# Performance work log

Measured on AMD Instinct MI355X. Metric: run time of the kernel, lower is better.

Reference implementation:

```python
import jax, jax.numpy as jnp
import numpy as np

EPS = 1e-5
AVG_D = 32.0


def setup_inputs() -> dict:
    key = jax.random.key(0)
    ks = jax.random.split(key, 12)
    Ns, Nd, E, D, K = 1_000_000, 100_000, 3_200_000, 16, 2
    Fs, Fd, V = 4, 4, 100_000
    F = Fd + K  # predictor fields
    inp = {}
    inp["Cat_src"] = jax.random.randint(ks[0], (Ns, Fs), 0, V)
    inp["Cat_dst"] = jax.random.randint(ks[1], (Nd, Fd), 0, V)
    inp["src_ids"] = jax.random.randint(ks[2], (E,), 0, Ns)
    inp["dst_ids"] = jax.random.randint(ks[3], (E,), 0, Nd)
    inp["label"] = jax.random.randint(ks[4], (Nd,), 0, 2)
    inp["w"] = jax.random.normal(ks[5], (V, D), dtype=jnp.float32) * 0.05
    inp["W_agg"] = jax.random.normal(ks[6], (K, 12 * D, D), dtype=jnp.float32) * 0.05
    inp["b_agg"] = jnp.zeros((K, D), jnp.float32)
    inp["w_lin"] = jax.random.normal(ks[7], (F * D,), dtype=jnp.float32) * 0.05
    inp["b_lin"] = jnp.zeros((1,), jnp.float32)
    inp["W1"] = jax.random.normal(ks[8], (F * D, 64), dtype=jnp.float32) * 0.05
    inp["b1"] = jnp.zeros((64,), jnp.float32)
    inp["W2"] = jax.random.normal(ks[9], (64, 32), dtype=jnp.float32) * 0.05
    inp["b2"] = jnp.zeros((32,), jnp.float32)
    inp["W3"] = jax.random.normal(ks[10], (32, 1), dtype=jnp.float32) * 0.05
    inp["b3"] = jnp.zeros((1,), jnp.float32)
    return inp


def reference(Cat_src, Cat_dst, src_ids, dst_ids, label, w, W_agg, b_agg,
              w_lin, b_lin, W1, b1, W2, b2, W3, b3):
    Nd = Cat_dst.shape[0]
    # --- node embedding: gather cat fields, RowEmb with modes [mean, max] -> [Ns, K, D]
    emb = w[Cat_src]                                      # [Ns, Fs, D]
    h_src = jnp.stack([emb.mean(1), emb.max(1)], axis=1)  # [Ns, K, D]
    # --- multi-aggregator message passing (copy_u + segment min/max/mean, std via mean of h^2)
    m = h_src[src_ids]                                    # [E, K, D]
    deg = jax.ops.segment_sum(jnp.ones(src_ids.shape, m.dtype), dst_ids, Nd)
    safe = jnp.maximum(deg, 1.0)[:, None, None]
    mean = jax.ops.segment_sum(m, dst_ids, Nd) / safe
    mean2 = jax.ops.segment_sum(m * m, dst_ids, Nd) / safe
    has = (deg > 0)[:, None, None]
    mn = jnp.where(has, jax.ops.segment_min(m, dst_ids, Nd), 0.0)
    mx = jnp.where(has, jax.ops.segment_max(m, dst_ids, Nd), 0.0)
    std = jnp.sqrt(jax.nn.relu(mean2 - mean * mean) + EPS)
    tmp = jnp.concatenate([mean, mn, mx, std], axis=-1)   # [Nd, K, 4D]
    # --- PNA degree scalers: identity / amplification / attenuation
    logd = jnp.log(deg + 1.0)
    log_avg = jnp.log(AVG_D + 1.0)
    amp = (logd / log_avg)[:, None, None]
    att = jnp.where(logd > 0, log_avg / jnp.maximum(logd, EPS), 0.0)[:, None, None]
    scaled = jnp.concatenate([tmp, tmp * amp, tmp * att], axis=-1)  # [Nd, K, 12D]
    mes = jnp.einsum('nkf,kfd->nkd', scaled, W_agg) + b_agg          # [Nd, K, D]
    # --- final block: concat dst cat embeddings with aggregated messages
    x = jnp.concatenate([w[Cat_dst], mes], axis=1)        # [Nd, F, D]
    # --- DeepFM predictor: linear + FM pairwise + deep MLP
    flat = x.reshape(Nd, -1)
    lin = flat @ w_lin + b_lin[0]
    s = x.sum(1)
    fm = 0.5 * ((s * s) - (x * x).sum(1)).sum(-1)
    h = jax.nn.relu(flat @ W1 + b1)
    h = jax.nn.relu(h @ W2 + b2)
    deep = (h @ W3 + b3)[:, 0]
    pred = jax.nn.sigmoid(lin + fm + deep)
    return (pred, label)
```

## Files before the change

### kernel.cpp

```cpp
#include <hip/hip_runtime.h>
#include <math.h>

#define EPSF 1e-5f
#define CAP  88
#define SBH  9
#define MAXSB 256
#define SBCAP 23552
#define TILE 4096
#define SEG  8
#define XPADS2 104
#define X2PADS 72
#define NPACK 14336

typedef __attribute__((ext_vector_type(8))) short short8;
typedef __attribute__((ext_vector_type(4))) float float4v;

__device__ inline unsigned f2bf_rne(float x) {
    unsigned u = __float_as_uint(x);
    u += 0x7FFF + ((u >> 16) & 1);
    return u >> 16;
}
__device__ inline short bf16_of(float x) { return (short)f2bf_rne(x); }
__device__ inline float bf2f_lo(unsigned hv) { return __uint_as_float(hv << 16); }
__device__ inline float bf2f_hi(unsigned hv) { return __uint_as_float(hv & 0xFFFF0000u); }
__device__ inline float bf2f_s(ushort s) { return __uint_as_float((unsigned)s << 16); }

__global__ __launch_bounds__(256) void setup_all(
    int* sbcursor, int* deg, int Nd, int nsb,
    const float* __restrict__ W_agg, const float* __restrict__ W1,
    const float* __restrict__ W2, ushort* __restrict__ wpack,
    const float* __restrict__ w, ushort* __restrict__ wb, int VD, int do_cast)
{
    int nzc = (Nd + 255) >> 8;
    int bid = blockIdx.x;
    if (bid < nzc) {
        int i = bid * 256 + threadIdx.x;
        if (i < Nd) deg[i] = 0;
        if (bid == 0 && threadIdx.x < nsb) sbcursor[threadIdx.x] = threadIdx.x * SBCAP;
        return;
    }
    if (bid == nzc) {
        for (int it = threadIdx.x; it < 1792; it += 256) {
            if (it < 768) {
                int t_g = it >> 6; int rem = it & 63;
                int q = rem >> 4, col = rem & 15;
                int kvar = t_g / 6, t = t_g % 6;
                const float* src = W_agg + kvar * 3072 + (t * 32 + q * 8) * 16 + col;
                ushort* dst = wpack + (size_t)it * 8;
#pragma unroll
                for (int j = 0; j < 8; ++j) dst[j] = (ushort)f2bf_rne(src[j * 16]);
            } else if (it < 1536) {
                int i2 = it - 768;
                int t = i2 >> 8; int rem = i2 & 255;
                int q = rem >> 6, col = rem & 63;
                const float* src = W1 + (t * 32 + q * 8) * 64 + col;
                ushort* dst = wpack + 6144 + (size_t)i2 * 8;
#pragma unroll
                for (int j = 0; j < 8; ++j) dst[j] = (ushort)f2bf_rne(src[j * 64]);
            } else {
                int i2 = it - 1536;
                int t = i2 >> 7; int rem = i2 & 127;
                int q = rem >> 5, col = rem & 31;
                const float* src = W2 + (t * 32 + q * 8) * 32 + col;
                ushort* dst = wpack + 12288 + (size_t)i2 * 8;
#pragma unroll
                for (int j = 0; j < 8; ++j) dst[j] = (ushort)f2bf_rne(src[j * 32]);
            }
        }
        return;
    }
    if (!do_cast) return;
    int i4 = ((bid - nzc - 1) * 256 + threadIdx.x) * 4;
    if (i4 + 3 < VD) {
        float4 v = *(const float4*)(w + i4);
        ushort4 o;
        o.x = (ushort)f2bf_rne(v.x); o.y = (ushort)f2bf_rne(v.y);
        o.z = (ushort)f2bf_rne(v.z); o.w = (ushort)f2bf_rne(v.w);
        *(ushort4*)(wb + i4) = o;
    } else {
        for (int j = i4; j < VD; ++j) wb[j] = (ushort)f2bf_rne(w[j]);
    }
}

__global__ __launch_bounds__(256) void build_h(
    const int* __restrict__ Cat_src, const ushort* __restrict__ wb,
    unsigned* __restrict__ h, int Ns)
{
    int gid = blockIdx.x * 256 + threadIdx.x;
    int s = gid >> 4;
    if (s >= Ns) return;
    int lane = threadIdx.x & 63;
    int d = lane & 15;
    int c = Cat_src[s * 4 + (d & 3)];
    float vs = 0.f, vm = -INFINITY;
#pragma unroll
    for (int f = 0; f < 4; ++f) {
        int id = __shfl(c, (lane & 48) + f, 64);
        float a = bf2f_s(wb[id * 16 + d]);
        vs += a; vm = fmaxf(vm, a);
    }
    unsigned packed = f2bf_rne(vs * 0.25f) | (f2bf_rne(vm) << 16);
    __builtin_nontemporal_store(packed, &h[s * 16 + d]);
}

__global__ __launch_bounds__(256) void scatter_sb(
    const int* __restrict__ src_ids, const int* __restrict__ dst_ids,
    int* sbcursor, unsigned* __restrict__ pairs1, int E, int nsb)
{
    __shared__ int cnt[MAXSB];
    __shared__ int base[MAXSB];
    int tid = threadIdx.x;
    int t0 = blockIdx.x * TILE;
    for (int i = tid; i < nsb; i += 256) cnt[i] = 0;
    __syncthreads();
    int rank[TILE / 256];
#pragma unroll
    for (int j = 0; j < TILE / 256; ++j) {
        int e = t0 + j * 256 + tid;
        rank[j] = (e < E) ? atomicAdd(&cnt[dst_ids[e] >> SBH], 1) : 0;
    }
    __syncthreads();
    for (int i = tid; i < nsb; i += 256) {
        int c = cnt[i];
        base[i] = c ? atomicAdd(&sbcursor[i], c) : 0;
    }
    __syncthreads();
#pragma unroll
    for (int j = 0; j < TILE / 256; ++j) {
        int e = t0 + j * 256 + tid;
        if (e < E) {
            int d = dst_ids[e];
            int sb = d >> SBH;
            int idx = base[sb] + rank[j];
            if (idx < (sb + 1) * SBCAP)
                pairs1[idx] = ((unsigned)src_ids[e] << 9) | (unsigned)(d & 511);
        }
    }
}

__global__ __launch_bounds__(256) void scatter_fine3(
    const unsigned* __restrict__ pairs1, const int* __restrict__ sbcursor,
    unsigned* __restrict__ pairs2, int* __restrict__ deg, int Nd, int nsb,
    int nsbp)
{
    __shared__ int cnt[512];
    __shared__ int base[512];
    int S = blockIdx.x % nsbp, seg = blockIdx.x / nsbp;
    if (S >= nsb) return;
    int tid = threadIdx.x;
    int sbs = S * SBCAP;
    int sbe = sbcursor[S];
    if (sbe > sbs + SBCAP) sbe = sbs + SBCAP;
    int len = sbe - sbs;
    int per = (len + SEG - 1) / SEG;
    int s0 = sbs + seg * per;
    int s1 = s0 + per; if (s1 > sbe) s1 = sbe;
    cnt[tid] = 0; cnt[tid + 256] = 0;
    __syncthreads();
    int rank[12];
    unsigned pv[12];
    int nit = (s1 - s0 + 255) >> 8;
    if (nit > 12) nit = 12;
    for (int j = 0; j < nit; ++j) {
        int e = s0 + j * 256 + tid;
        if (e < s1) {
            unsigned p = __builtin_nontemporal_load(&pairs1[e]);
            pv[j] = p;
            rank[j] = atomicAdd(&cnt[p & 511u], 1);
        }
    }
    __syncthreads();
#pragma unroll
    for (int r = 0; r < 2; ++r) {
        int l = tid + r * 256;
        int c = cnt[l];
        int gdst = (S << 9) + l;
        base[l] = (c && gdst < Nd) ? atomicAdd(&deg[gdst], c) : 0;
    }
    __syncthreads();
    for (int j = 0; j < nit; ++j) {
        int e = s0 + j * 256 + tid;
        if (e < s1) {
            unsigned p = pv[j];
            int l = (int)(p & 511u);
            int idx = base[l] + rank[j];
            if (idx < CAP)
                pairs2[(size_t)((S << 9) + l) * CAP + idx] = p >> 9;
        }
    }
}

__device__ inline void emit_stats(float sum0, float sq0, float mn0, float mx0,
                                  float sum1, float sq1, float mn1, float mx1,
                                  int dg, int n, int lane, int sub,
                                  ushort* __restrict__ tmpb)
{
#pragma unroll
    for (int off = 16; off <= 32; off <<= 1) {
        sum0 += __shfl_xor(sum0, off); sq0 += __shfl_xor(sq0, off);
        mn0 = fminf(mn0, __shfl_xor(mn0, off)); mx0 = fmaxf(mx0, __shfl_xor(mx0, off));
        sum1 += __shfl_xor(sum1, off); sq1 += __shfl_xor(sq1, off);
        mn1 = fminf(mn1, __shfl_xor(mn1, off)); mx1 = fmaxf(mx1, __shfl_xor(mx1, off));
    }
    float safe = fmaxf((float)dg, 1.f);
    float r = 1.f / safe;
    bool has = dg > 0;
    float mean0 = sum0 * r, mean1 = sum1 * r;
    float sd0 = sqrtf(fmaxf(sq0 * r - mean0 * mean0, 0.f) + EPSF);
    float sd1 = sqrtf(fmaxf(sq1 * r - mean1 * mean1, 0.f) + EPSF);
    float v0 = (sub == 0) ? mean0 : (sub == 1) ? (has ? mn0 : 0.f)
             : (sub == 2) ? (has ? mx0 : 0.f) : sd0;
    float v1 = (sub == 0) ? mean1 : (sub == 1) ? (has ? mn1 : 0.f)
             : (sub == 2) ? (has ? mx1 : 0.f) : sd1;
    ushort* tp = tmpb + (size_t)n * 128;
    tp[lane] = (ushort)f2bf_rne(v0);
    tp[64 + lane] = (ushort)f2bf_rne(v1);
}

#define ACC8(HV)  do { \
    float me = bf2f_lo(HV); \
    float vm = bf2f_hi(HV); \
    sum0 += me; sq0 += me * me; \
    mn0 = fminf(mn0, me); mx0 = fmaxf(mx0, me); \
    sum1 += vm; sq1 += vm * vm; \
    mn1 = fminf(mn1, vm); mx1 = fmaxf(mx1, vm); } while (0)

__global__ __launch_bounds__(256) void agg_from_h2(
    const unsigned* __restrict__ h, const int* __restrict__ deg,
    const unsigned* __restrict__ pairs,
    ushort* __restrict__ tmpb, int Nd)
{
    int tid = threadIdx.x;
    int wv = tid >> 6, lane = tid & 63, sub = lane >> 4, d = lane & 15;
    int n = blockIdx.x * 4 + wv;
    if (n >= Nd) return;
    int dg = deg[n];
    int dgc = (dg < CAP) ? dg : CAP;
    const unsigned* pw = pairs + (size_t)n * CAP;

    float sum0 = 0.f, sq0 = 0.f, mn0 = INFINITY, mx0 = -INFINITY;
    float sum1 = 0.f, sq1 = 0.f, mn1 = INFINITY, mx1 = -INFINITY;

    int t64 = dgc >> 6;
    for (int t = 0; t < t64; ++t) {
        const unsigned* pp = pw + t * 64 + sub;
        unsigned pv[16], hv[16];
#pragma unroll
        for (int j = 0; j < 16; ++j) pv[j] = pp[j * 4];
#pragma unroll
        for (int j = 0; j < 16; ++j) hv[j] = h[pv[j] * 16 + d];
#pragma unroll
        for (int j = 0; j < 16; ++j) ACC8(hv[j]);
    }
    int base = t64 << 6;
    if (dgc & 32) {
        const unsigned* pp = pw + base + sub;
        unsigned pv[8], hv[8];
#pragma unroll
        for (int j = 0; j < 8; ++j) pv[j] = pp[j * 4];
#pragma unroll
        for (int j = 0; j < 8; ++j) hv[j] = h[pv[j] * 16 + d];
#pragma unroll
        for (int j = 0; j < 8; ++j) ACC8(hv[j]);
        base += 32;
    }
    int rem = dgc - base;
    if (rem > 0) {
        int last = dgc - 1;
        unsigned pv[8], hv[8];
#pragma unroll
        for (int j = 0; j < 8; ++j) {
            if (j * 4 < rem) {
                int e = base + j * 4 + sub;
                pv[j] = pw[e < last ? e : last];
            }
        }
#pragma unroll
        for (int j = 0; j < 8; ++j)
            if (j * 4 < rem) hv[j] = h[pv[j] * 16 + d];
#pragma unroll
        for (int j = 0; j < 8; ++j) {
            if (j * 4 < rem) {
                if (base + j * 4 + sub < dgc) ACC8(hv[j]);
            }
        }
    }
    emit_stats(sum0, sq0, mn0, mx0, sum1, sq1, mn1, mx1,
               dg, n, lane, sub, tmpb);
}

__global__ __launch_bounds__(256) void agg_from_w2(
    const int* __restrict__ Cat_src, const float* __restrict__ w,
    const ushort* __restrict__ wb, int use_bf,
    const int* __restrict__ deg, const unsigned* __restrict__ pairs,
    ushort* __restrict__ tmpb, int Nd)
{
    int tid = threadIdx.x;
    int wv = tid >> 6, lane = tid & 63, sub = lane >> 4, d = lane & 15;
    int n = blockIdx.x * 4 + wv;
    if (n >= Nd) return;
    int dg = deg[n];
    int dgc = (dg < CAP) ? dg : CAP;
    const unsigned* pw = pairs + (size_t)n * CAP;

    float sum0 = 0.f, sq0 = 0.f, mn0 = INFINITY, mx0 = -INFINITY;
    float sum1 = 0.f, sq1 = 0.f, mn1 = INFINITY, mx1 = -INFINITY;
    int nt = (dgc + 3) >> 2;
    for (int t = 0; t < nt; ++t) {
        int e4 = t * 4 + sub;
        int ec = (e4 < dgc) ? e4 : (dgc - 1);
        int src = (int)pw[ec];
        int cat = Cat_src[src * 4 + (d & 3)];
        float vs = 0.f, vm = -INFINITY;
        if (use_bf) {
#pragma unroll
            for (int f = 0; f < 4; ++f) {
                int id = __shfl(cat, sub * 16 + f, 64);
                float a = bf2f_s(wb[id * 16 + d]);
                vs += a; vm = fmaxf(vm, a);
            }
        } else {
#pragma unroll
            for (int f = 0; f < 4; ++f) {
                int id = __shfl(cat, sub * 16 + f, 64);
                float a = w[id * 16 + d];
                vs += a; vm = fmaxf(vm, a);
            }
        }
        if (e4 < dgc) {
            float me = vs * 0.25f;
            sum0 += me; sq0 += me * me;
            mn0 = fminf(mn0, me); mx0 = fmaxf(mx0, me);
            sum1 += vm; sq1 += vm * vm;
            mn1 = fminf(mn1, vm); mx1 = fmaxf(mx1, vm);
        }
    }
    emit_stats(sum0, sq0, mn0, mx0, sum1, sq1, mn1, mx1,
               dg, n, lane, sub, tmpb);
}

__global__ __launch_bounds__(256) void finalize_mfma(
    const int* __restrict__ Cat_dst, const int* __restrict__ label,
    const float* __restrict__ w, const ushort* __restrict__ wpack,
    const float* __restrict__ b_agg,
    const float* __restrict__ w_lin, const float* __restrict__ b_lin,
    const float* __restrict__ b1, const float* __restrict__ b2,
    const float* __restrict__ W3, const float* __restrict__ b3,
    const int* __restrict__ deg_arr, const ushort* __restrict__ tmpb,
    float* __restrict__ out, int Nd)
{
    __shared__ __align__(16) ushort sx[4][16 * XPADS2];
    __shared__ __align__(16) ushort sx2[4][16 * X2PADS];
    __shared__ float sdeep[4][16];

    int tid = threadIdx.x;
    int wv = tid >> 6, lane = tid & 63;
    int q = lane >> 4, m = lane & 15;
    int n0 = (blockIdx.x * 4 + wv) * 16;
    int n = n0 + m;
    int nc = (n < Nd) ? n : (Nd - 1);

    ushort* X = sx[wv];
    ushort* X2 = sx2[wv];

    float fdeg = (float)deg_arr[nc];
    float logd = logf(fdeg + 1.f);
    const float logavg = logf(33.0f);
    float amp = logd / logavg;
    float att = (logd > 0.f) ? (logavg / fmaxf(logd, EPSF)) : 0.f;
    float ampr[4], attr[4];
#pragma unroll
    for (int r = 0; r < 4; ++r) {
        ampr[r] = __shfl(amp, q * 4 + r, 64);
        attr[r] = __shfl(att, q * 4 + r, 64);
    }

    const ushort* tpn = tmpb + (size_t)nc * 128;
#pragma unroll
    for (int kvar = 0; kvar < 2; ++kvar) {
        short8 af0 = *(const short8*)(tpn + kvar * 64 + q * 8);
        short8 af1 = *(const short8*)(tpn + kvar * 64 + 32 + q * 8);
        float4v aI = {0.f,0.f,0.f,0.f}, aA = {0.f,0.f,0.f,0.f}, aT = {0.f,0.f,0.f,0.f};
#pragma unroll
        for (int sb = 0; sb < 3; ++sb) {
            short8 b0 = *(const short8*)(wpack +
                (size_t)(((kvar * 6 + sb * 2) * 4 + q) * 16 + m) * 8);
            short8 b1v = *(const short8*)(wpack +
                (size_t)(((kvar * 6 + sb * 2 + 1) * 4 + q) * 16 + m) * 8);
            if (sb == 0) {
                aI = __builtin_amdgcn_mfma_f32_16x16x32_bf16(af0, b0, aI, 0, 0, 0);
                aI = __builtin_amdgcn_mfma_f32_16x16x32_bf16(af1, b1v, aI, 0, 0, 0);
            } else if (sb == 1) {
                aA = __builtin_amdgcn_mfma_f32_16x16x32_bf16(af0, b0, aA, 0, 0, 0);
                aA = __builtin_amdgcn_mfma_f32_16x16x32_bf16(af1, b1v, aA, 0, 0, 0);
            } else {
                aT = __builtin_amdgcn_mfma_f32_16x16x32_bf16(af0, b0, aT, 0, 0, 0);
                aT = __builtin_amdgcn_mfma_f32_16x16x32_bf16(af1, b1v, aT, 0, 0, 0);
            }
        }
        float bias = b_agg[kvar * 16 + m];
#pragma unroll
        for (int r = 0; r < 4; ++r)
            X[(q * 4 + r) * XPADS2 + 64 + kvar * 16 + m] = (ushort)f2bf_rne(
                aI[r] + ampr[r] * aA[r] + attr[r] * aT[r] + bias);
    }
    {
        int nl = lane >> 2, fl = lane & 3;
        int nn = n0 + nl;
        int nnc = (nn < Nd) ? nn : (Nd - 1);
        int cid = Cat_dst[nnc * 4 + fl];
        const float4* R = (const float4*)(w + (size_t)cid * 16);
        float4 r0 = R[0], r1 = R[1], r2 = R[2], r3 = R[3];
        short8 o0, o1;
        o0[0] = bf16_of(r0.x); o0[1] = bf16_of(r0.y);
        o0[2] = bf16_of(r0.z); o0[3] = bf16_of(r0.w);
        o0[4] = bf16_of(r1.x); o0[5] = bf16_of(r1.y);
        o0[6] = bf16_of(r1.z); o0[7] = bf16_of(r1.w);
        o1[0] = bf16_of(r2.x); o1[1] = bf16_of(r2.y);
        o1[2] = bf16_of(r2.z); o1[3] = bf16_of(r2.w);
        o1[4] = bf16_of(r3.x); o1[5] = bf16_of(r3.y);
        o1[6] = bf16_of(r3.z); o1[7] = bf16_of(r3.w);
        ushort* xp = X + nl * XPADS2 + fl * 16;
        *(short8*)(xp) = o0;
        *(short8*)(xp + 8) = o1;
    }
    __syncthreads();

    float lin = 0.f, sq = 0.f;
    float sd[16];
#pragma unroll
    for (int u = 0; u < 16; ++u) sd[u] = 0.f;
    {
        const ushort* xp = X + m * XPADS2 + q * 16;
        const float* wl = w_lin + q * 16;
#pragma unroll
        for (int u = 0; u < 16; ++u) {
            float v = bf2f_s(xp[u]);
            lin += v * wl[u]; sq += v * v; sd[u] += v;
        }
    }
    if (q < 2) {
        const ushort* xp = X + m * XPADS2 + (4 + q) * 16;
        const float* wl = w_lin + (4 + q) * 16;
#pragma unroll
        for (int u = 0; u < 16; ++u) {
            float v = bf2f_s(xp[u]);
            lin += v * wl[u]; sq += v * v; sd[u] += v;
        }
    }
#pragma unroll
    for (int off = 16; off <= 32; off <<= 1) {
        lin += __shfl_xor(lin, off);
        sq  += __shfl_xor(sq, off);
#pragma unroll
        for (int u = 0; u < 16; ++u) sd[u] += __shfl_xor(sd[u], off);
    }
    float fm = 0.f;
#pragma unroll
    for (int u = 0; u < 16; ++u) fm += sd[u] * sd[u];
    fm = 0.5f * (fm - sq);

    short8 xa[3];
#pragma unroll
    for (int t = 0; t < 3; ++t)
        xa[t] = *(const short8*)(X + m * XPADS2 + t * 32 + q * 8);
#pragma unroll
    for (int nt = 0; nt < 4; ++nt) {
        float4v acc = {0.f, 0.f, 0.f, 0.f};
#pragma unroll
        for (int t = 0; t < 3; ++t) {
            short8 bf = *(const short8*)(wpack + 6144 +
                (size_t)((t * 4 + q) * 64 + nt * 16 + m) * 8);
            acc = __builtin_amdgcn_mfma_f32_16x16x32_bf16(xa[t], bf, acc, 0, 0, 0);
        }
        float bb = b1[nt * 16 + m];
#pragma unroll
        for (int r = 0; r < 4; ++r)
            X2[(q * 4 + r) * X2PADS + nt * 16 + m] =
                (ushort)f2bf_rne(fmaxf(acc[r] + bb, 0.f));
    }
    __syncthreads();

    short8 ha[2];
#pragma unroll
    for (int t = 0; t < 2; ++t)
        ha[t] = *(const short8*)(X2 + m * X2PADS + t * 32 + q * 8);
    float dp[4] = {0.f, 0.f, 0.f, 0.f};
#pragma unroll
    for (int nt = 0; nt < 2; ++nt) {
        float4v acc = {0.f, 0.f, 0.f, 0.f};
#pragma unroll
        for (int t = 0; t < 2; ++t) {
            short8 bf = *(const short8*)(wpack + 12288 +
                (size_t)((t * 4 + q) * 32 + nt * 16 + m) * 8);
            acc = __builtin_amdgcn_mfma_f32_16x16x32_bf16(ha[t], bf, acc, 0, 0, 0);
        }
        float bb = b2[nt * 16 + m];
        float w3 = W3[nt * 16 + m];
#pragma unroll
        for (int r = 0; r < 4; ++r)
            dp[r] += fmaxf(acc[r] + bb, 0.f) * w3;
    }
#pragma unroll
    for (int off = 1; off <= 8; off <<= 1) {
#pragma unroll
        for (int r = 0; r < 4; ++r) dp[r] += __shfl_xor(dp[r], off);
    }
    if (m < 4)
        sdeep[wv][q * 4 + m] = (m == 0) ? dp[0] : (m == 1) ? dp[1]
                             : (m == 2) ? dp[2] : dp[3];
    __syncthreads();
    float deep = sdeep[wv][m];

    if (q == 0 && n < Nd) {
        float z = lin + b_lin[0] + fm + deep + b3[0];
        float pred = 1.f / (1.f + expf(-z));
        out[n] = pred;
        out[Nd + n] = (float)label[n];
    }
}

extern "C" void kernel_launch(void* const* d_in, const int* in_sizes, int n_in,
                              void* d_out, int out_size, void* d_ws, size_t ws_size,
                              hipStream_t stream) {
    const int*   Cat_src = (const int*)d_in[0];
    const int*   Cat_dst = (const int*)d_in[1];
    const int*   src_ids = (const int*)d_in[2];
    const int*   dst_ids = (const int*)d_in[3];
    const int*   label   = (const int*)d_in[4];
    const float* w       = (const float*)d_in[5];
    const float* W_agg   = (const float*)d_in[6];
    const float* b_agg   = (const float*)d_in[7];
    const float* w_lin   = (const float*)d_in[8];
    const float* b_lin   = (const float*)d_in[9];
    const float* W1      = (const float*)d_in[10];
    const float* b1      = (const float*)d_in[11];
    const float* W2      = (const float*)d_in[12];
    const float* b2      = (const float*)d_in[13];
    const float* W3      = (const float*)d_in[14];
    const float* b3      = (const float*)d_in[15];

    int E  = in_sizes[2];
    int Nd = in_sizes[4];
    int Ns = in_sizes[0] / 4;
    int VD = in_sizes[5];
    int nsb = (Nd + (1 << SBH) - 1) >> SBH;
    int nsbp = (nsb + 7) & ~7;

    int* sbcursor = (int*)d_ws;
    int* deg      = sbcursor + MAXSB;
    size_t off_p2 = (((size_t)(MAXSB + Nd)) * 4 + 255) & ~(size_t)255;
    unsigned* pairs2 = (unsigned*)((char*)d_ws + off_p2);
    size_t off_u = (off_p2 + (size_t)Nd * CAP * 4 + 255) & ~(size_t)255;
    unsigned* pairs1 = (unsigned*)((char*)d_ws + off_u);
    ushort*   tmpb   = (ushort*)((char*)d_ws + off_u);
    size_t u_p1 = (size_t)nsb * SBCAP * 4;
    size_t u_tm = (size_t)Nd * 256;
    size_t u_bytes = (u_p1 > u_tm) ? u_p1 : u_tm;
    size_t off_w = (off_u + u_bytes + 255) & ~(size_t)255;
    ushort* wpack  = (ushort*)((char*)d_ws + off_w);
    ushort* w_bf16 = wpack + NPACK;
    unsigned* h    = (unsigned*)(w_bf16 + VD);

    size_t need_common = off_w + (size_t)NPACK * 2;
    size_t need_A = need_common + (size_t)VD * 2;
    size_t need_B = need_A + (size_t)Ns * 64;
    int mode = (ws_size >= need_B) ? 2 : (ws_size >= need_A) ? 1 : 0;

    float* out = (float*)d_out;

    int nzc = (Nd + 255) >> 8;
    int ncb = (mode >= 1) ? (VD / 4 + 255) / 256 : 0;
    hipLaunchKernelGGL(setup_all, dim3(nzc + 1 + ncb), dim3(256), 0, stream,
                       sbcursor, deg, Nd, nsb, W_agg, W1, W2, wpack,
                       w, w_bf16, VD, mode >= 1);
    if (mode == 2) {
        int hb = (int)(((size_t)Ns * 16 + 255) / 256);
        hipLaunchKernelGGL(build_h, dim3(hb), dim3(256), 0, stream,
                           Cat_src, w_bf16, h, Ns);
    }
    hipLaunchKernelGGL(scatter_sb, dim3((E + TILE - 1) / TILE), dim3(256), 0, stream,
                       src_ids, dst_ids, sbcursor, pairs1, E, nsb);
    hipLaunchKernelGGL(scatter_fine3, dim3(nsbp * SEG), dim3(256), 0, stream,
                       pairs1, sbcursor, pairs2, deg, Nd, nsb, nsbp);
    int nab = (Nd + 3) >> 2;
    if (mode == 2) {
        hipLaunchKernelGGL(agg_from_h2, dim3(nab), dim3(256), 0, stream,
                           h, deg, pairs2, tmpb, Nd);
    } else {
        hipLaunchKernelGGL(agg_from_w2, dim3(nab), dim3(256), 0, stream,
                           Cat_src, w, w_bf16, mode, deg, pairs2, tmpb, Nd);
    }
    hipLaunchKernelGGL(finalize_mfma, dim3((Nd + 63) / 64), dim3(256), 0, stream,
                       Cat_dst, label, w, wpack, b_agg, w_lin, b_lin,
                       b1, b2, W3, b3, deg, tmpb, out, Nd);
}
```

Baseline: 316.7 us.

## Shard superblock cursors, vectorize edge scatter and per-node h build

The coarse edge scatter now keeps eight cursors per superblock, one shard per block index mod 8. The fine scatter reads each shard's range directly instead of splitting the superblock evenly, and edge ids are loaded as int4 with a smaller tile. build_h has one thread per source node loading whole 16-element bf16 rows with vector loads and vector stores, and the aggregation inner loop drops from 64-edge to 32-edge batches. These aim to cut atomic contention on the global cursors and raise memory-access width, at the cost of overflow if one shard holds more than an eighth of a superblock's capacity.

New measurement: 295.6 us. 1.07x faster.

```diff
diff --git a/kernel.cpp b/kernel.cpp
--- a/kernel.cpp
+++ b/kernel.cpp
@@ -6,7 +6,8 @@
 #define SBH  9
 #define MAXSB 256
 #define SBCAP 23552
-#define TILE 4096
+#define SHCAP (SBCAP / 8)
+#define TILE 2048
 #define SEG  8
 #define XPADS2 104
 #define X2PADS 72
@@ -14,6 +15,7 @@
 
 typedef __attribute__((ext_vector_type(8))) short short8;
 typedef __attribute__((ext_vector_type(4))) float float4v;
+typedef __attribute__((ext_vector_type(4))) unsigned uint4v;
 
 __device__ inline unsigned f2bf_rne(float x) {
     unsigned u = __float_as_uint(x);
@@ -36,7 +38,13 @@
     if (bid < nzc) {
         int i = bid * 256 + threadIdx.x;
         if (i < Nd) deg[i] = 0;
-        if (bid == 0 && threadIdx.x < nsb) sbcursor[threadIdx.x] = threadIdx.x * SBCAP;
+        if (bid == 0) {
+            for (int j = threadIdx.x; j < 8 * MAXSB; j += 256) {
+                int s = j >> 8;
+                int sb = j & (MAXSB - 1);
+                sbcursor[j] = sb * SBCAP + s * SHCAP;
+            }
+        }
         return;
     }
     if (bid == nzc) {
@@ -82,25 +90,45 @@
     }
 }
 
-__global__ __launch_bounds__(256) void build_h(
+__global__ __launch_bounds__(256) void build_h2(
     const int* __restrict__ Cat_src, const ushort* __restrict__ wb,
     unsigned* __restrict__ h, int Ns)
 {
-    int gid = blockIdx.x * 256 + threadIdx.x;
-    int s = gid >> 4;
+    int s = blockIdx.x * 256 + threadIdx.x;
     if (s >= Ns) return;
-    int lane = threadIdx.x & 63;
-    int d = lane & 15;
-    int c = Cat_src[s * 4 + (d & 3)];
-    float vs = 0.f, vm = -INFINITY;
-#pragma unroll
-    for (int f = 0; f < 4; ++f) {
-        int id = __shfl(c, (lane & 48) + f, 64);
-        float a = bf2f_s(wb[id * 16 + d]);
-        vs += a; vm = fmaxf(vm, a);
-    }
-    unsigned packed = f2bf_rne(vs * 0.25f) | (f2bf_rne(vm) << 16);
-    __builtin_nontemporal_store(packed, &h[s * 16 + d]);
+    int4 c = *(const int4*)(Cat_src + (size_t)s * 4);
+    const short8* r0 = (const short8*)(wb + (size_t)c.x * 16);
+    const short8* r1 = (const short8*)(wb + (size_t)c.y * 16);
+    const short8* r2 = (const short8*)(wb + (size_t)c.z * 16);
+    const short8* r3 = (const short8*)(wb + (size_t)c.w * 16);
+    short8 a0 = r0[0], b0 = r0[1];
+    short8 a1 = r1[0], b1 = r1[1];
+    short8 a2 = r2[0], b2 = r2[1];
+    short8 a3 = r3[0], b3 = r3[1];
+    uint4v o0, o1, o2, o3;
+#pragma unroll
+    for (int d = 0; d < 8; ++d) {
+        float v0 = bf2f_s((ushort)a0[d]), v1 = bf2f_s((ushort)a1[d]);
+        float v2 = bf2f_s((ushort)a2[d]), v3 = bf2f_s((ushort)a3[d]);
+        float mean = (v0 + v1 + v2 + v3) * 0.25f;
+        float mx = fmaxf(fmaxf(v0, v1), fmaxf(v2, v3));
+        unsigned pk = f2bf_rne(mean) | (f2bf_rne(mx) << 16);
+        if (d < 4) o0[d] = pk; else o1[d - 4] = pk;
+    }
+#pragma unroll
+    for (int d = 0; d < 8; ++d) {
+        float v0 = bf2f_s((ushort)b0[d]), v1 = bf2f_s((ushort)b1[d]);
+        float v2 = bf2f_s((ushort)b2[d]), v3 = bf2f_s((ushort)b3[d]);
+        float mean = (v0 + v1 + v2 + v3) * 0.25f;
+        float mx = fmaxf(fmaxf(v0, v1), fmaxf(v2, v3));
+        unsigned pk = f2bf_rne(mean) | (f2bf_rne(mx) << 16);
+        if (d < 4) o2[d] = pk; else o3[d - 4] = pk;
+    }
+    uint4v* hp = (uint4v*)(h + (size_t)s * 16);
+    __builtin_nontemporal_store(o0, hp);
+    __builtin_nontemporal_store(o1, hp + 1);
+    __builtin_nontemporal_store(o2, hp + 2);
+    __builtin_nontemporal_store(o3, hp + 3);
 }
 
 __global__ __launch_bounds__(256) void scatter_sb(
@@ -111,34 +139,67 @@
     __shared__ int base[MAXSB];
     int tid = threadIdx.x;
     int t0 = blockIdx.x * TILE;
+    int shard = blockIdx.x & 7;
     for (int i = tid; i < nsb; i += 256) cnt[i] = 0;
     __syncthreads();
-    int rank[TILE / 256];
-#pragma unroll
-    for (int j = 0; j < TILE / 256; ++j) {
-        int e = t0 + j * 256 + tid;
-        rank[j] = (e < E) ? atomicAdd(&cnt[dst_ids[e] >> SBH], 1) : 0;
+    int dj[2][4];
+    int rank[2][4];
+#pragma unroll
+    for (int j = 0; j < 2; ++j) {
+        int e4 = t0 + (j * 256 + tid) * 4;
+        if (e4 + 3 < E) {
+            int4 dd = *(const int4*)(dst_ids + e4);
+            dj[j][0] = dd.x; dj[j][1] = dd.y; dj[j][2] = dd.z; dj[j][3] = dd.w;
+#pragma unroll
+            for (int k = 0; k < 4; ++k)
+                rank[j][k] = atomicAdd(&cnt[dj[j][k] >> SBH], 1);
+        } else {
+#pragma unroll
+            for (int k = 0; k < 4; ++k) {
+                int e = e4 + k;
+                dj[j][k] = (e < E) ? dst_ids[e] : 0;
+                rank[j][k] = (e < E) ? atomicAdd(&cnt[dj[j][k] >> SBH], 1) : 0;
+            }
+        }
     }
     __syncthreads();
     for (int i = tid; i < nsb; i += 256) {
         int c = cnt[i];
-        base[i] = c ? atomicAdd(&sbcursor[i], c) : 0;
-    }
-    __syncthreads();
-#pragma unroll
-    for (int j = 0; j < TILE / 256; ++j) {
-        int e = t0 + j * 256 + tid;
-        if (e < E) {
-            int d = dst_ids[e];
-            int sb = d >> SBH;
-            int idx = base[sb] + rank[j];
-            if (idx < (sb + 1) * SBCAP)
-                pairs1[idx] = ((unsigned)src_ids[e] << 9) | (unsigned)(d & 511);
-        }
-    }
-}
-
-__global__ __launch_bounds__(256) void scatter_fine3(
+        base[i] = c ? atomicAdd(&sbcursor[shard * MAXSB + i], c) : 0;
+    }
+    __syncthreads();
+#pragma unroll
+    for (int j = 0; j < 2; ++j) {
+        int e4 = t0 + (j * 256 + tid) * 4;
+        if (e4 + 3 < E) {
+            int4 sv = *(const int4*)(src_ids + e4);
+            int sj[4] = {sv.x, sv.y, sv.z, sv.w};
+#pragma unroll
+            for (int k = 0; k < 4; ++k) {
+                int d = dj[j][k];
+                int sb = d >> SBH;
+                int idx = base[sb] + rank[j][k];
+                if (idx < sb * SBCAP + (shard + 1) * SHCAP)
+                    pairs1[idx] = ((unsigned)sj[k] << 9) | (unsigned)(d & 511);
+            }
+        } else {
+#pragma unroll
+            for (int k = 0; k < 4; ++k) {
+                int e = e4 + k;
+                if (e < E) {
+                    int d = dj[j][k];
+                    int sb = d >> SBH;
+                    int idx = base[sb] + rank[j][k];
+                    if (idx < sb * SBCAP + (shard + 1) * SHCAP)
+                        pairs1[idx] = ((unsigned)src_ids[e] << 9)
+                                    | (unsigned)(d & 511);
+                }
+            }
+        }
+    }
+}
+
+__global__ __launch_bounds__(256) void scatter_fine4(
     const unsigned* __restrict__ pairs1, const int* __restrict__ sbcursor,
     unsigned* __restrict__ pairs2, int* __restrict__ deg, int Nd, int nsb,
     int nsbp)
@@ -148,13 +209,9 @@
     int S = blockIdx.x % nsbp, seg = blockIdx.x / nsbp;
     if (S >= nsb) return;
     int tid = threadIdx.x;
-    int sbs = S * SBCAP;
-    int sbe = sbcursor[S];
-    if (sbe > sbs + SBCAP) sbe = sbs + SBCAP;
-    int len = sbe - sbs;
-    int per = (len + SEG - 1) / SEG;
-    int s0 = sbs + seg * per;
-    int s1 = s0 + per; if (s1 > sbe) s1 = sbe;
+    int s0 = S * SBCAP + seg * SHCAP;
+    int s1 = sbcursor[seg * MAXSB + S];
+    if (s1 > s0 + SHCAP) s1 = s0 + SHCAP;
     cnt[tid] = 0; cnt[tid + 256] = 0;
     __syncthreads();
     int rank[12];
@@ -217,14 +274,6 @@
     tp[64 + lane] = (ushort)f2bf_rne(v1);
 }
 
-#define ACC8(HV)  do { \
-    float me = bf2f_lo(HV); \
-    float vm = bf2f_hi(HV); \
-    sum0 += me; sq0 += me * me; \
-    mn0 = fminf(mn0, me); mx0 = fmaxf(mx0, me); \
-    sum1 += vm; sq1 += vm * vm; \
-    mn1 = fminf(mn1, vm); mx1 = fmaxf(mx1, vm); } while (0)
-
 __global__ __launch_bounds__(256) void agg_from_h2(
     const unsigned* __restrict__ h, const int* __restrict__ deg,
     const unsigned* __restrict__ pairs,
@@ -241,29 +290,25 @@
     float sum0 = 0.f, sq0 = 0.f, mn0 = INFINITY, mx0 = -INFINITY;
     float sum1 = 0.f, sq1 = 0.f, mn1 = INFINITY, mx1 = -INFINITY;
 
-    int t64 = dgc >> 6;
-    for (int t = 0; t < t64; ++t) {
-        const unsigned* pp = pw + t * 64 + sub;
-        unsigned pv[16], hv[16];
-#pragma unroll
-        for (int j = 0; j < 16; ++j) pv[j] = pp[j * 4];
-#pragma unroll
-        for (int j = 0; j < 16; ++j) hv[j] = h[pv[j] * 16 + d];
-#pragma unroll
-        for (int j = 0; j < 16; ++j) ACC8(hv[j]);
-    }
-    int base = t64 << 6;
-    if (dgc & 32) {
-        const unsigned* pp = pw + base + sub;
+    int nfull = dgc >> 5;
+    for (int t = 0; t < nfull; ++t) {
+        const unsigned* pp = pw + t * 32 + sub;
         unsigned pv[8], hv[8];
 #pragma unroll
         for (int j = 0; j < 8; ++j) pv[j] = pp[j * 4];
 #pragma unroll
         for (int j = 0; j < 8; ++j) hv[j] = h[pv[j] * 16 + d];
 #pragma unroll
-        for (int j = 0; j < 8; ++j) ACC8(hv[j]);
-        base += 32;
-    }
+        for (int j = 0; j < 8; ++j) {
+            float me = bf2f_lo(hv[j]);
+            float vm = bf2f_hi(hv[j]);
+            sum0 += me; sq0 += me * me;
+            mn0 = fminf(mn0, me); mx0 = fmaxf(mx0, me);
+            sum1 += vm; sq1 += vm * vm;
+            mn1 = fminf(mn1, vm); mx1 = fmaxf(mx1, vm);
+        }
+    }
+    int base = nfull << 5;
     int rem = dgc - base;
     if (rem > 0) {
         int last = dgc - 1;
@@ -281,7 +326,14 @@
 #pragma unroll
         for (int j = 0; j < 8; ++j) {
             if (j * 4 < rem) {
-                if (base + j * 4 + sub < dgc) ACC8(hv[j]);
+                if (base + j * 4 + sub < dgc) {
+                    float me = bf2f_lo(hv[j]);
+                    float vm = bf2f_hi(hv[j]);
+                    sum0 += me; sq0 += me * me;
+                    mn0 = fminf(mn0, me); mx0 = fmaxf(mx0, me);
+                    sum1 += vm; sq1 += vm * vm;
+                    mn1 = fminf(mn1, vm); mx1 = fmaxf(mx1, vm);
+                }
             }
         }
     }
@@ -309,7 +361,7 @@
     for (int t = 0; t < nt; ++t) {
         int e4 = t * 4 + sub;
         int ec = (e4 < dgc) ? e4 : (dgc - 1);
-        int src = (int)pw[ec];
+        int src = (dgc > 0) ? (int)pw[ec] : 0;
         int cat = Cat_src[src * 4 + (d & 3)];
         float vs = 0.f, vm = -INFINITY;
         if (use_bf) {
@@ -548,8 +600,8 @@
     int nsbp = (nsb + 7) & ~7;
 
     int* sbcursor = (int*)d_ws;
-    int* deg      = sbcursor + MAXSB;
-    size_t off_p2 = (((size_t)(MAXSB + Nd)) * 4 + 255) & ~(size_t)255;
+    int* deg      = sbcursor + 8 * MAXSB;
+    size_t off_p2 = (((size_t)(8 * MAXSB + Nd)) * 4 + 255) & ~(size_t)255;
     unsigned* pairs2 = (unsigned*)((char*)d_ws + off_p2);
     size_t off_u = (off_p2 + (size_t)Nd * CAP * 4 + 255) & ~(size_t)255;
     unsigned* pairs1 = (unsigned*)((char*)d_ws + off_u);
@@ -575,13 +627,13 @@
                        sbcursor, deg, Nd, nsb, W_agg, W1, W2, wpack,
                        w, w_bf16, VD, mode >= 1);
     if (mode == 2) {
-        int hb = (int)(((size_t)Ns * 16 + 255) / 256);
-        hipLaunchKernelGGL(build_h, dim3(hb), dim3(256), 0, stream,
+        int hb = (Ns + 255) / 256;
+        hipLaunchKernelGGL(build_h2, dim3(hb), dim3(256), 0, stream,
                            Cat_src, w_bf16, h, Ns);
     }
     hipLaunchKernelGGL(scatter_sb, dim3((E + TILE - 1) / TILE), dim3(256), 0, stream,
                        src_ids, dst_ids, sbcursor, pairs1, E, nsb);
-    hipLaunchKernelGGL(scatter_fine3, dim3(nsbp * SEG), dim3(256), 0, stream,
+    hipLaunchKernelGGL(scatter_fine4, dim3(nsbp * SEG), dim3(256), 0, stream,
                        pairs1, sbcursor, pairs2, deg, Nd, nsb, nsbp);
     int nab = (Nd + 3) >> 2;
     if (mode == 2) {
```
